# Kernel tuning notes

Hardware: AMD Instinct MI355X
Metric: run time of the kernel (lower is better)

Reference implementation:

```python
import jax, jax.numpy as jnp
import numpy as np

EMBED_DIM = 512
NUM_HEADS = 8
HEAD_DIM = EMBED_DIM // NUM_HEADS
SCALING = HEAD_DIM ** -0.5
T, B = 2048, 4
NEG_INF = -1e9


def setup_inputs() -> dict:
    key = jax.random.key(0)
    k1, k2, k3 = jax.random.split(key, 3)
    h = jax.random.normal(k1, (T, B, EMBED_DIM), dtype=jnp.float32)
    # causal additive mask, [T, T]: 0 on/below diagonal, -inf above
    attn_mask = jnp.where(jnp.triu(jnp.ones((T, T), dtype=bool), k=1), NEG_INF, 0.0).astype(jnp.float32)
    in_proj_weight = jax.random.normal(k2, (3 * EMBED_DIM, EMBED_DIM), dtype=jnp.float32) * 0.02
    in_proj_bias = jnp.zeros((3 * EMBED_DIM,), dtype=jnp.float32)
    out_w = jax.random.normal(k3, (EMBED_DIM, EMBED_DIM), dtype=jnp.float32) * 0.02
    out_b = jnp.zeros((EMBED_DIM,), dtype=jnp.float32)
    return {"h": h, "attn_mask": attn_mask, "in_proj_weight": in_proj_weight,
            "in_proj_bias": in_proj_bias, "out_w": out_w, "out_b": out_b}


def reference(h, attn_mask, in_proj_weight, in_proj_bias, out_w, out_b):
    tgt_len, bsz, embed_dim = h.shape
    # fused QKV projection: [T, B, 3E]
    qkv = jnp.einsum('tbe,fe->tbf', h, in_proj_weight) + in_proj_bias
    q, k, v = jnp.split(qkv, 3, axis=-1)
    q = q * SCALING
    # [T, B, E] -> [B*H, T, hd]
    def to_heads(x):
        return x.reshape(tgt_len, bsz * NUM_HEADS, HEAD_DIM).transpose(1, 0, 2)
    q, k, v = to_heads(q), to_heads(k), to_heads(v)
    # scores: [B*H, T, S]
    attn_weights = jnp.einsum('bth,bsh->bts', q, k)
    attn_weights = attn_weights + attn_mask[None, :, :]
    attn_p = jax.nn.softmax(attn_weights, axis=-1)
    attn = jnp.einsum('bts,bsh->bth', attn_p, v)
    # [B*H, T, hd] -> [T, B, E]
    attn = attn.transpose(1, 0, 2).reshape(tgt_len, bsz, embed_dim)
    out = jnp.einsum('tbe,fe->tbf', attn, out_w) + out_b
    return out, attn_p.reshape(bsz, NUM_HEADS, tgt_len, tgt_len)
```

## Files before the change

### kernel.cpp

```cpp
#include <hip/hip_runtime.h>
#include <cstdint>
#include <cstddef>

#define T_SEQ 2048
#define BSZ 4
#define EMB 512
#define NH 8
#define HD 64
#define SCALING 0.125f
#define NEGBIG (-1e30f)
#define PW 144

typedef short bf16x8_t __attribute__((ext_vector_type(8)));
typedef float f32x4_t __attribute__((ext_vector_type(4)));
typedef short short4v __attribute__((ext_vector_type(4)));
typedef float float4v __attribute__((ext_vector_type(4)));

typedef __attribute__((address_space(1))) const void* as1_cvp;
typedef __attribute__((address_space(3))) void* as3_vp;

#define MFMA16(a, b, c) __builtin_amdgcn_mfma_f32_16x16x32_bf16((a), (b), (c), 0, 0, 0)

static __device__ __forceinline__ short f2b(float f) {
  union { float f; uint32_t u; } x; x.f = f;
  uint32_t r = (x.u + 0x7fffu + ((x.u >> 16) & 1u)) >> 16;
  return (short)(r & 0xffffu);
}

static __device__ __forceinline__ void gload_lds16(const void* g, void* l) {
  __builtin_amdgcn_global_load_lds((as1_cvp)g, (as3_vp)l, 16, 0, 0);
}

__global__ __launch_bounds__(256) void cvt_kernel(const float* __restrict__ in,
                                                  short* __restrict__ out) {
  int i = (blockIdx.x * 256 + threadIdx.x) * 4;
  float4v v = *(const float4v*)(in + i);
  short4v o;
  o[0] = f2b(v[0]); o[1] = f2b(v[1]); o[2] = f2b(v[2]); o[3] = f2b(v[3]);
  *(short4v*)(out + i) = o;
}

template <int EPI>
__global__ __launch_bounds__(256)
void gemm_bt(const short* __restrict__ A, const short* __restrict__ Bt,
             const float* __restrict__ bias,
             short* __restrict__ outQ, short* __restrict__ outK, short* __restrict__ outV,
             float* __restrict__ outF) {
  __shared__ short ldsA[128 * 32];
  __shared__ short ldsB[128 * 32];
  const int tid = threadIdx.x;
  const int wid = tid >> 6, lane = tid & 63, g = lane >> 4, r16 = lane & 15;
  const int wr = wid >> 1, wc = wid & 1;
  const int mbase = blockIdx.y * 128, nbase = blockIdx.x * 128;

  f32x4_t acc[4][4];
#pragma unroll
  for (int m = 0; m < 4; ++m)
#pragma unroll
    for (int n = 0; n < 4; ++n) acc[m][n] = (f32x4_t){0.f, 0.f, 0.f, 0.f};

  for (int kt = 0; kt < 16; ++kt) {
    __syncthreads();
#pragma unroll
    for (int i = 0; i < 2; ++i) {
      int c = i * 256 + tid;
      int row = c >> 2, j4 = c & 3;
      gload_lds16(A + (size_t)(mbase + row) * 512 + kt * 32 + j4 * 8, &ldsA[c * 8]);
      gload_lds16(Bt + (size_t)(nbase + row) * 512 + kt * 32 + j4 * 8, &ldsB[c * 8]);
    }
    __syncthreads();
    bf16x8_t af[4], bfv[4];
#pragma unroll
    for (int m = 0; m < 4; ++m)
      af[m] = *(const bf16x8_t*)&ldsA[(wr * 64 + m * 16 + r16) * 32 + g * 8];
#pragma unroll
    for (int n = 0; n < 4; ++n)
      bfv[n] = *(const bf16x8_t*)&ldsB[(wc * 64 + n * 16 + r16) * 32 + g * 8];
#pragma unroll
    for (int m = 0; m < 4; ++m)
#pragma unroll
      for (int n = 0; n < 4; ++n) acc[m][n] = MFMA16(af[m], bfv[n], acc[m][n]);
  }

#pragma unroll
  for (int m = 0; m < 4; ++m) {
#pragma unroll
    for (int n = 0; n < 4; ++n) {
      int col = nbase + wc * 64 + n * 16 + r16;
      float bcol = bias[col];
#pragma unroll
      for (int j = 0; j < 4; ++j) {
        int row = mbase + wr * 64 + m * 16 + g * 4 + j;
        float v = acc[m][n][j] + bcol;
        if (EPI == 0) {
          int sect = col >> 9, e = col & 511, hh = e >> 6, d = e & 63;
          int t = row >> 2, b = row & 3;
          size_t dst = ((size_t)(b * NH + hh) * T_SEQ + t) * HD + d;
          short bv = f2b(v);
          if (sect == 0) outQ[dst] = bv;
          else if (sect == 1) outK[dst] = bv;
          else outV[dst] = bv;
        } else {
          outF[(size_t)row * EMB + col] = v;
        }
      }
    }
  }
}

__global__ __launch_bounds__(256)
void attn_fused(const short* __restrict__ Qg, const short* __restrict__ Kg,
                const short* __restrict__ Vg, float* __restrict__ Pout,
                short* __restrict__ attnO) {
  __shared__ __align__(16) short lds[26624];
  short* Kt = lds;
  short* Vt = lds + 8192;
  short(*Pl)[16 * PW] = (short(*)[16 * PW])(lds + 8192 + 9216);
  const int bh = blockIdx.x;
  const int qt = 31 - (int)blockIdx.y;
  const int tid = threadIdx.x, wid = tid >> 6, lane = tid & 63;
  const int g = lane >> 4, r16 = lane & 15;
  const size_t headOff = (size_t)bh * T_SEQ * HD;
  const int wrow0 = qt * 64 + wid * 16;
  const int myrow = wrow0 + r16;
  const int maxcol = qt * 64 + 64;
  const int nt128 = (qt >> 1) + 1;
  const short* Kh = Kg + headOff;
  const short* Vh = Vg + headOff;

  bf16x8_t qf[2];
  {
    const short* qp = Qg + headOff + (size_t)myrow * HD + g * 8;
    qf[0] = *(const bf16x8_t*)qp;
    qf[1] = *(const bf16x8_t*)(qp + 32);
  }

  float m_w = NEGBIG;
  float m_t = NEGBIG;
  float l_w = 0.f;
  f32x4_t oacc[4];
#pragma unroll
  for (int dc = 0; dc < 4; ++dc) oacc[dc] = (f32x4_t){0.f, 0.f, 0.f, 0.f};

  uint32_t* Vtu = (uint32_t*)Vt;
  const int kp0 = tid & 63, dg0 = tid >> 6;

  bf16x8_t va[2], vb[2];
#define VLOAD(KB)                                                              \
  {                                                                            \
    const short* vp0 = Vh + (size_t)((KB) + kp0 * 2) * HD + dg0 * 8;           \
    va[0] = *(const bf16x8_t*)vp0; vb[0] = *(const bf16x8_t*)(vp0 + HD);       \
    const short* vp1 = vp0 + 32;                                               \
    va[1] = *(const bf16x8_t*)vp1; vb[1] = *(const bf16x8_t*)(vp1 + HD);       \
  }
  VLOAD(0)

  for (int kt = 0; kt < nt128; ++kt) {
    const int kb = kt * 128;
    __syncthreads();
#pragma unroll
    for (int i = 0; i < 4; ++i) {
      int cc = i * 256 + tid;
      int row = cc >> 3, j8 = (cc & 7) ^ (row & 7);
      gload_lds16(Kh + (size_t)(kb + row) * HD + j8 * 8, &Kt[cc * 8]);
    }
#pragma unroll
    for (int i = 0; i < 2; ++i) {
      int dg = dg0 + i * 4;
#pragma unroll
      for (int j = 0; j < 8; ++j)
        Vtu[(dg * 8 + j) * (PW / 2) + kp0] =
            (uint32_t)(uint16_t)va[i][j] | ((uint32_t)(uint16_t)vb[i][j] << 16);
    }
    __syncthreads();
    if (kt + 1 < nt128) VLOAD(kb + 128)
    const int H = ((maxcol - kb) >= 128) ? 2 : 1;
#pragma unroll
    for (int h = 0; h < 2; ++h) {
      if (h < H) {
        float sv[4][4];
#pragma unroll
        for (int kc4 = 0; kc4 < 4; ++kc4) {
          const int rl = (h * 4 + kc4) * 16 + r16;
          f32x4_t s = {0.f, 0.f, 0.f, 0.f};
#pragma unroll
          for (int kk = 0; kk < 2; ++kk) {
            int byteo = (rl * 128 + kk * 64 + g * 16) ^ ((rl & 7) << 4);
            bf16x8_t kf = *(const bf16x8_t*)((const char*)Kt + byteo);
            s = MFMA16(kf, qf[kk], s);
          }
          const int key0 = kb + (h * 4 + kc4) * 16 + g * 4;
#pragma unroll
          for (int j = 0; j < 4; ++j)
            sv[kc4][j] = (key0 + j <= myrow) ? s[j] * SCALING : NEGBIG;
        }
        float pm = NEGBIG;
#pragma unroll
        for (int kc4 = 0; kc4 < 4; ++kc4)
#pragma unroll
          for (int j = 0; j < 4; ++j) pm = fmaxf(pm, sv[kc4][j]);
        m_t = fmaxf(m_t, pm);
#pragma unroll
        for (int off = 1; off < 64; off <<= 1) pm = fmaxf(pm, __shfl_xor(pm, off));
        float mn = fmaxf(m_w, pm);
        if (mn > m_w + 8.f) {
          float sc = __expf(m_w - mn);
          l_w *= sc;
#pragma unroll
          for (int dc = 0; dc < 4; ++dc)
#pragma unroll
            for (int j = 0; j < 4; ++j) oacc[dc][j] *= sc;
          m_w = mn;
        }
#pragma unroll
        for (int kc4 = 0; kc4 < 4; ++kc4) {
          short4v pb;
#pragma unroll
          for (int j = 0; j < 4; ++j) {
            float e = __expf(sv[kc4][j] - m_w);
            l_w += e;
            pb[j] = f2b(e);
          }
          *(short4v*)&Pl[wid][r16 * PW + (h * 4 + kc4) * 16 + g * 4] = pb;
        }
#pragma unroll
        for (int kk2 = 0; kk2 < 2; ++kk2) {
          const int kc2 = h * 2 + kk2;
          bf16x8_t pf = *(const bf16x8_t*)&Pl[wid][r16 * PW + kc2 * 32 + g * 8];
#pragma unroll
          for (int dc = 0; dc < 4; ++dc) {
            bf16x8_t vf = *(const bf16x8_t*)&Vt[(dc * 16 + r16) * PW + kc2 * 32 + g * 8];
            oacc[dc] = MFMA16(pf, vf, oacc[dc]);
          }
        }
      }
    }
  }

#pragma unroll
  for (int off = 16; off <= 32; off <<= 1) {
    m_t = fmaxf(m_t, __shfl_xor(m_t, off));
    l_w += __shfl_xor(l_w, off);
  }
  const float m_row = m_t;
  const float rl2 = __expf(m_row - m_w) / l_w;

  float lo[4];
#pragma unroll
  for (int j = 0; j < 4; ++j) lo[j] = 1.0f / __shfl(l_w, g * 4 + j);
#pragma unroll
  for (int dc = 0; dc < 4; ++dc) {
#pragma unroll
    for (int j = 0; j < 4; ++j) {
      int t = wrow0 + g * 4 + j, d = dc * 16 + r16;
      size_t ntok = (size_t)t * BSZ + (bh >> 3);
      attnO[ntok * EMB + (bh & 7) * HD + d] = f2b(oacc[dc][j] * lo[j]);
    }
  }

  short* Kb0 = lds;
  short* Kb1 = lds + 8192;
  float* Prow = Pout + ((size_t)bh * T_SEQ + myrow) * T_SEQ;

#define STAGEK(KB, BUF)                                                        \
  {                                                                            \
    _Pragma("unroll")                                                          \
    for (int i = 0; i < 4; ++i) {                                              \
      int cc = i * 256 + tid;                                                  \
      int row = cc >> 3, j8 = (cc & 7) ^ (row & 7);                            \
      gload_lds16(Kh + (size_t)((KB) + row) * HD + j8 * 8, &(BUF)[cc * 8]);    \
    }                                                                          \
  }

  __syncthreads();
  STAGEK(0, Kb0)
  __syncthreads();
  int p = 0;
  for (int kt = 0; kt < nt128; ++kt) {
    const int kb = kt * 128;
    short* cur = p ? Kb1 : Kb0;
    short* nxt = p ? Kb0 : Kb1;
    if (kt + 1 < nt128) STAGEK(kb + 128, nxt)
    const int navail = (maxcol - kb) >> 4;
    const int nkc = navail < 8 ? navail : 8;
#pragma unroll
    for (int kc = 0; kc < 8; ++kc) {
      if (kc < nkc) {
        const int rl = kc * 16 + r16;
        f32x4_t s = {0.f, 0.f, 0.f, 0.f};
#pragma unroll
        for (int kk = 0; kk < 2; ++kk) {
          int byteo = (rl * 128 + kk * 64 + g * 16) ^ ((rl & 7) << 4);
          bf16x8_t kf = *(const bf16x8_t*)((const char*)cur + byteo);
          s = MFMA16(kf, qf[kk], s);
        }
        const int key0 = kb + kc * 16 + g * 4;
        float4v pvv;
#pragma unroll
        for (int j = 0; j < 4; ++j) {
          float e = __expf(s[j] * SCALING - m_row) * rl2;
          pvv[j] = (key0 + j <= myrow) ? e : 0.f;
        }
        *(float4v*)(Prow + key0) = pvv;
      }
    }
    __syncthreads();
    p ^= 1;
  }

  const int c0 = maxcol;
  const int nc4 = (T_SEQ - c0) >> 2;
  for (int r = 0; r < 64; ++r) {
    size_t base = ((size_t)bh * T_SEQ + qt * 64 + r) * T_SEQ + c0;
    for (int c4 = tid; c4 < nc4; c4 += 256) {
      float4v z = {0.f, 0.f, 0.f, 0.f};
      *(float4v*)(Pout + base + (size_t)c4 * 4) = z;
    }
  }
}

extern "C" void kernel_launch(void* const* d_in, const int* in_sizes, int n_in,
                              void* d_out, int out_size, void* d_ws, size_t ws_size,
                              hipStream_t stream) {
  const float* h = (const float*)d_in[0];
  const float* w_in = (const float*)d_in[2];
  const float* b_in = (const float*)d_in[3];
  const float* w_out = (const float*)d_in[4];
  const float* b_out = (const float*)d_in[5];
  float* out = (float*)d_out;
  float* Pout = out + (size_t)T_SEQ * BSZ * EMB;

  short* hB = (short*)d_ws;
  short* wB = hB + (size_t)8192 * 512;
  short* owB = wB + (size_t)1536 * 512;
  short* qB = owB + (size_t)512 * 512;
  short* kB = qB + (size_t)32 * 2048 * 64;
  short* vB = kB + (size_t)32 * 2048 * 64;
  short* aB = vB + (size_t)32 * 2048 * 64;

  cvt_kernel<<<4096, 256, 0, stream>>>(h, hB);
  cvt_kernel<<<768, 256, 0, stream>>>(w_in, wB);
  cvt_kernel<<<256, 256, 0, stream>>>(w_out, owB);

  gemm_bt<0><<<dim3(12, 64), 256, 0, stream>>>(hB, wB, b_in, qB, kB, vB, nullptr);
  attn_fused<<<dim3(32, 32), 256, 0, stream>>>(qB, kB, vB, Pout, aB);
  gemm_bt<1><<<dim3(4, 64), 256, 0, stream>>>(aB, owB, b_out, nullptr, nullptr, nullptr, out);
}
```

Baseline: 228.6 us.

## Write V transposed in QKV epilogue and read V fragments directly from global

The QKV projection epilogue now writes V in a [head, dim, token] layout. The attention kernel loads its PV-MFMA operands straight from global memory instead of staging and transposing V through LDS each key tile. This removes the per-tile V register prefetch, the LDS transpose writes and some LDS capacity, and the P scratch row pitch shrinks. In exchange, the epilogue V stores become strided with stride T_SEQ, the MFMA operands now depend on global/L2 latency inside the inner loop, and the new pitch makes P rows no longer 16-byte aligned for vector LDS reads.

```diff
diff --git a/kernel.cpp b/kernel.cpp
--- a/kernel.cpp
+++ b/kernel.cpp
@@ -9,7 +9,7 @@
 #define HD 64
 #define SCALING 0.125f
 #define NEGBIG (-1e30f)
-#define PW 144
+#define PW 132
 
 typedef short bf16x8_t __attribute__((ext_vector_type(8)));
 typedef float f32x4_t __attribute__((ext_vector_type(4)));
@@ -95,11 +95,11 @@
         if (EPI == 0) {
           int sect = col >> 9, e = col & 511, hh = e >> 6, d = e & 63;
           int t = row >> 2, b = row & 3;
-          size_t dst = ((size_t)(b * NH + hh) * T_SEQ + t) * HD + d;
+          int bh = b * NH + hh;
           short bv = f2b(v);
-          if (sect == 0) outQ[dst] = bv;
-          else if (sect == 1) outK[dst] = bv;
-          else outV[dst] = bv;
+          if (sect == 0) outQ[((size_t)bh * T_SEQ + t) * HD + d] = bv;
+          else if (sect == 1) outK[((size_t)bh * T_SEQ + t) * HD + d] = bv;
+          else outV[((size_t)bh * HD + d) * T_SEQ + t] = bv;
         } else {
           outF[(size_t)row * EMB + col] = v;
         }
@@ -110,12 +110,11 @@
 
 __global__ __launch_bounds__(256)
 void attn_fused(const short* __restrict__ Qg, const short* __restrict__ Kg,
-                const short* __restrict__ Vg, float* __restrict__ Pout,
+                const short* __restrict__ VTg, float* __restrict__ Pout,
                 short* __restrict__ attnO) {
-  __shared__ __align__(16) short lds[26624];
+  __shared__ __align__(16) short lds[8192 + 4 * 16 * PW];
   short* Kt = lds;
-  short* Vt = lds + 8192;
-  short(*Pl)[16 * PW] = (short(*)[16 * PW])(lds + 8192 + 9216);
+  short(*Pl)[16 * PW] = (short(*)[16 * PW])(lds + 8192);
   const int bh = blockIdx.x;
   const int qt = 31 - (int)blockIdx.y;
   const int tid = threadIdx.x, wid = tid >> 6, lane = tid & 63;
@@ -126,7 +125,7 @@
   const int maxcol = qt * 64 + 64;
   const int nt128 = (qt >> 1) + 1;
   const short* Kh = Kg + headOff;
-  const short* Vh = Vg + headOff;
+  const short* VTh = VTg + headOff;
 
   bf16x8_t qf[2];
   {
@@ -142,19 +141,6 @@
 #pragma unroll
   for (int dc = 0; dc < 4; ++dc) oacc[dc] = (f32x4_t){0.f, 0.f, 0.f, 0.f};
 
-  uint32_t* Vtu = (uint32_t*)Vt;
-  const int kp0 = tid & 63, dg0 = tid >> 6;
-
-  bf16x8_t va[2], vb[2];
-#define VLOAD(KB)                                                              \
-  {                                                                            \
-    const short* vp0 = Vh + (size_t)((KB) + kp0 * 2) * HD + dg0 * 8;           \
-    va[0] = *(const bf16x8_t*)vp0; vb[0] = *(const bf16x8_t*)(vp0 + HD);       \
-    const short* vp1 = vp0 + 32;                                               \
-    va[1] = *(const bf16x8_t*)vp1; vb[1] = *(const bf16x8_t*)(vp1 + HD);       \
-  }
-  VLOAD(0)
-
   for (int kt = 0; kt < nt128; ++kt) {
     const int kb = kt * 128;
     __syncthreads();
@@ -164,16 +150,7 @@
       int row = cc >> 3, j8 = (cc & 7) ^ (row & 7);
       gload_lds16(Kh + (size_t)(kb + row) * HD + j8 * 8, &Kt[cc * 8]);
     }
-#pragma unroll
-    for (int i = 0; i < 2; ++i) {
-      int dg = dg0 + i * 4;
-#pragma unroll
-      for (int j = 0; j < 8; ++j)
-        Vtu[(dg * 8 + j) * (PW / 2) + kp0] =
-            (uint32_t)(uint16_t)va[i][j] | ((uint32_t)(uint16_t)vb[i][j] << 16);
-    }
-    __syncthreads();
-    if (kt + 1 < nt128) VLOAD(kb + 128)
+    __syncthreads();
     const int H = ((maxcol - kb) >= 128) ? 2 : 1;
 #pragma unroll
     for (int h = 0; h < 2; ++h) {
@@ -229,7 +206,8 @@
           bf16x8_t pf = *(const bf16x8_t*)&Pl[wid][r16 * PW + kc2 * 32 + g * 8];
 #pragma unroll
           for (int dc = 0; dc < 4; ++dc) {
-            bf16x8_t vf = *(const bf16x8_t*)&Vt[(dc * 16 + r16) * PW + kc2 * 32 + g * 8];
+            bf16x8_t vf = *(const bf16x8_t*)(VTh + (size_t)(dc * 16 + r16) * T_SEQ +
+                                             kb + kc2 * 32 + g * 8);
             oacc[dc] = MFMA16(pf, vf, oacc[dc]);
           }
         }
@@ -259,7 +237,7 @@
   }
 
   short* Kb0 = lds;
-  short* Kb1 = lds + 8192;
+  short* Kb1 = (short*)Pl;
   float* Prow = Pout + ((size_t)bh * T_SEQ + myrow) * T_SEQ;
 
 #define STAGEK(KB, BUF)                                                        \
```

Measured after the change: 241.0 us. 1.05x slower.
